# Kernel tuning notes

Hardware: AMD Instinct MI355X
Metric: run time of the kernel (lower is better)

Reference implementation:

```python
import jax, jax.numpy as jnp
import numpy as np
from jax import lax

N_CLASS, EMB, HID = 32000, 512, 1024
BATCH, SEQ = 64, 256


def _run_lstm(xs, h0, c0, Wg, Wgh, bg, Wi, Wih, bi, Wf, Wfh, bf, Wo, Woh, bo):
    # xs: [T, B, D_in]; weights stored [D_in, H] so step is x @ W (== Linear)
    def step(carry, x):
        h, c = carry
        g = jnp.tanh(x @ Wg + h @ Wgh + bg)
        i = jax.nn.sigmoid(x @ Wi + h @ Wih + bi)
        f = jax.nn.sigmoid(x @ Wf + h @ Wfh + bf)
        o = jax.nn.sigmoid(x @ Wo + h @ Woh + bo)
        c = c * f + g * i
        h = jnp.tanh(c) * o
        return (h, c), h
    (hT, cT), hs = lax.scan(step, (h0, c0), xs)
    return hs, hT


def setup_inputs() -> dict:
    key = jax.random.key(0)
    ks = jax.random.split(key, 32)
    s_e, s_h = 1.0 / np.sqrt(EMB), 1.0 / np.sqrt(HID)
    d = {}
    d["X"] = jax.random.randint(ks[0], (BATCH, SEQ), 0, N_CLASS)
    d["C"] = jax.random.normal(ks[1], (N_CLASS, EMB), jnp.float32)
    # layer 1 (input dim EMB)
    names1 = ["W1", "W_xi", "W_xf", "W_xo"]
    names1h = ["W2", "W_hi", "W_hf", "W_ho"]
    for j, n in enumerate(names1):
        d[n] = jax.random.normal(ks[2 + j], (EMB, HID), jnp.float32) * s_e
    for j, n in enumerate(names1h):
        d[n] = jax.random.normal(ks[6 + j], (HID, HID), jnp.float32) * s_h
    for n in ["b1", "b_i", "b_f", "b_o"]:
        d[n] = jnp.ones((HID,), jnp.float32)
    # layer 2 (input dim HID)
    names2 = ["W1_y", "W_xi_y", "W_xf_y", "W_xo_y", "W2_y", "W_hi_y", "W_hf_y", "W_ho_y"]
    for j, n in enumerate(names2):
        d[n] = jax.random.normal(ks[10 + j], (HID, HID), jnp.float32) * s_h
    for n in ["b1_y", "b_i_y", "b_f_y", "b_o_y"]:
        d[n] = jnp.ones((HID,), jnp.float32)
    d["W3"] = jax.random.normal(ks[20], (HID, N_CLASS), jnp.float32) * s_h
    d["b2"] = jnp.ones((N_CLASS,), jnp.float32)
    # torch code uses torch.randn initial states each call; materialize them
    d["h0"] = jax.random.normal(ks[21], (BATCH, HID), jnp.float32)
    d["c0"] = jax.random.normal(ks[22], (BATCH, HID), jnp.float32)
    d["h0_y"] = jax.random.normal(ks[23], (BATCH, HID), jnp.float32)
    d["c0_y"] = jax.random.normal(ks[24], (BATCH, HID), jnp.float32)
    return d


def reference(X, C, W1, W_xi, W_xf, W_xo, W2, W_hi, W_hf, W_ho,
              b1, b_i, b_f, b_o,
              W1_y, W_xi_y, W_xf_y, W_xo_y, W2_y, W_hi_y, W_hf_y, W_ho_y,
              b1_y, b_i_y, b_f_y, b_o_y, W3, b2, h0, c0, h0_y, c0_y):
    xs = jnp.transpose(C[X], (1, 0, 2))  # [T, B, EMB]
    hs, _ = _run_lstm(xs, h0, c0, W1, W2, b1, W_xi, W_hi, b_i,
                      W_xf, W_hf, b_f, W_xo, W_ho, b_o)
    _, hT_y = _run_lstm(hs, h0_y, c0_y, W1_y, W2_y, b1_y, W_xi_y, W_hi_y, b_i_y,
                        W_xf_y, W_hf_y, b_f_y, W_xo_y, W_ho_y, b_o_y)
    return hT_y @ W3 + b2  # [B, N_CLASS]
```

## Files before the change

kernel.cpp:

```cpp
#include <hip/hip_runtime.h>
#include <hip/hip_bf16.h>


typedef __attribute__((ext_vector_type(8))) short s16x8;
typedef __attribute__((ext_vector_type(4))) float f32x4;
typedef unsigned long long u64;

#define N_CLASS 32000
#define EMB 512
#define HID 1024
#define BATCH 64
#define SEQ 256
#define NG4 4096

#define PIN(v) asm volatile("" : "+v"(v))

static __device__ __forceinline__ short f2bf(float x) {
  __hip_bfloat16 h = __float2bfloat16(x);
  return *reinterpret_cast<short*>(&h);
}
static __device__ __forceinline__ float bf2f(short x) {
  __hip_bfloat16 h = *reinterpret_cast<__hip_bfloat16*>(&x);
  return __bfloat162float(h);
}
static __device__ __forceinline__ float fsigm(float x) {
  return __builtin_amdgcn_rcpf(1.f + __expf(-x));
}
static __device__ __forceinline__ float ftanh(float x) {
  return 2.f * __builtin_amdgcn_rcpf(1.f + __expf(-2.f * x)) - 1.f;
}

__global__ void k_conv_w4(const float* __restrict__ Wg, const float* __restrict__ Wi,
                          const float* __restrict__ Wf, const float* __restrict__ Wo,
                          short* __restrict__ sw, int K) {
  int i = blockIdx.x * 256 + threadIdx.x;
  int k8 = i >> 10, j = i & 1023;
  if (k8 >= (K >> 3)) return;
  const float* W = blockIdx.z == 0 ? Wg : blockIdx.z == 1 ? Wi : blockIdx.z == 2 ? Wf : Wo;
  s16x8 v;
#pragma unroll
  for (int e = 0; e < 8; ++e) v[e] = f2bf(W[(size_t)(k8 * 8 + e) * 1024 + j]);
  *(s16x8*)(sw + ((size_t)k8 * NG4 + blockIdx.z * 1024 + j) * 8) = v;
}

__global__ void k_bcat(const float* __restrict__ b0, const float* __restrict__ b1,
                       const float* __restrict__ b2, const float* __restrict__ b3,
                       float* __restrict__ dst) {
  int i = blockIdx.x * 256 + threadIdx.x;
  const float* s = (i >> 10) == 0 ? b0 : (i >> 10) == 1 ? b1 : (i >> 10) == 2 ? b2 : b3;
  dst[i] = s[i & 1023];
}

__global__ void k_f2bf(const float* __restrict__ src, short* __restrict__ dst, int n) {
  int i = blockIdx.x * 256 + threadIdx.x;
  if (i < n) dst[i] = f2bf(src[i]);
}

__global__ void k_embed(const int* __restrict__ X, const float* __restrict__ C,
                        short* __restrict__ xs) {
  int r = blockIdx.x;
  int t = r >> 6, b = r & 63;
  int idx = X[b * SEQ + t];
  const float* src = C + (size_t)idx * EMB;
  float2 v = *(const float2*)(src + threadIdx.x * 2);
  short* dst = xs + (size_t)r * EMB + threadIdx.x * 2;
  dst[0] = f2bf(v.x);
  dst[1] = f2bf(v.y);
}

__global__ __launch_bounds__(256) void k_gemx(const short* __restrict__ A,
                                              const short* __restrict__ Bsw,
                                              const float* __restrict__ bias,
                                              u64* __restrict__ Gsw) {
  __shared__ short lds[4096 * 8];
  int tid = threadIdx.x;
  int n0 = blockIdx.x * 64;
  for (int cid = tid; cid < 4096; cid += 256) {
    int k8 = cid >> 6, nl = cid & 63;
    *(s16x8*)(lds + (size_t)cid * 8) = *(const s16x8*)(Bsw + ((size_t)k8 * NG4 + n0 + nl) * 8);
  }
  __syncthreads();
  int lane = tid & 63, wid = tid >> 6;
  int l15 = lane & 15, l4 = lane >> 4;
  int ms = wid >> 1, ns = wid & 1;
  for (int m0 = blockIdx.y * 64; m0 < SEQ * BATCH; m0 += gridDim.y * 64) {
    f32x4 acc[2][2];
#pragma unroll
    for (int i = 0; i < 2; ++i)
#pragma unroll
      for (int j = 0; j < 2; ++j) acc[i][j] = (f32x4){0.f, 0.f, 0.f, 0.f};
    const short* a0p = A + (size_t)(m0 + ms * 32 + l15) * EMB + l4 * 8;
    const short* a1p = a0p + (size_t)16 * EMB;
#pragma unroll 4
    for (int kc = 0; kc < 16; ++kc) {
      s16x8 av0 = *(const s16x8*)(a0p + kc * 32);
      s16x8 av1 = *(const s16x8*)(a1p + kc * 32);
#pragma unroll
      for (int j = 0; j < 2; ++j) {
        s16x8 bv = *(const s16x8*)(lds + (size_t)((kc * 4 + l4) * 64 + ns * 32 + j * 16 + l15) * 8);
        acc[0][j] = __builtin_amdgcn_mfma_f32_16x16x32_bf16(av0, bv, acc[0][j], 0, 0, 0);
        acc[1][j] = __builtin_amdgcn_mfma_f32_16x16x32_bf16(av1, bv, acc[1][j], 0, 0, 0);
      }
    }
    int t = m0 >> 6;
#pragma unroll
    for (int i = 0; i < 2; ++i)
#pragma unroll
      for (int j = 0; j < 2; ++j) {
        int grp = ms * 2 + i;
        int colg = n0 + ns * 32 + j * 16 + l15;
        float bv = bias[colg];
        int q = colg >> 10, nslc = (colg >> 4) & 63;
        u64 pk = 0;
#pragma unroll
        for (int e = 0; e < 4; ++e)
          pk |= (u64)(unsigned short)f2bf(acc[i][j][e] + bv) << (16 * e);
        size_t slot = ((((size_t)t * 4 + grp) * 64 + nslc) * 4 + q) * 64 + l4 * 16 + l15;
        Gsw[slot] = pk;
      }
  }
}

__global__ __launch_bounds__(512, 2) void k_mega(
    const u64* __restrict__ G64, const short* __restrict__ Wh1sw,
    const short* __restrict__ Wx2sw, const short* __restrict__ Wh2sw,
    const float* __restrict__ bc2, u64* __restrict__ h1ex, u64* __restrict__ h2ex,
    const float* __restrict__ c0, const float* __restrict__ c0y,
    u64* __restrict__ hTy, unsigned* __restrict__ flags) {
  __shared__ short a_lds[2 * 16 * 1024];
  __shared__ f32x4 xch[8][64];
  const int tid = threadIdx.x;
  const int lane = tid & 63, W = tid >> 6;
  const int wv = W & 3, khalf = W >> 2;
  const int l15 = lane & 15, l4 = lane >> 4;
  const int xcd = (int)blockIdx.x & 7;
  const int idx = (int)blockIdx.x >> 3;
  const int group = idx & 3;
  const int nsl = ((idx >> 2) << 3) | xcd;
  const int col = (l15 >> 2) * 1024 + nsl * 16 + wv * 4 + (l15 & 3);

  s16x8 b1r[16], bxr[16], b2r[16];
#pragma unroll
  for (int j = 0; j < 16; ++j) {
    size_t o = ((size_t)((khalf * 16 + j) * 4 + l4) * NG4 + col) * 8;
    b1r[j] = *(const s16x8*)(Wh1sw + o);
    PIN(b1r[j]);
  }
#pragma unroll
  for (int j = 0; j < 16; ++j) {
    size_t o = ((size_t)((khalf * 16 + j) * 4 + l4) * NG4 + col) * 8;
    bxr[j] = *(const s16x8*)(Wx2sw + o);
    PIN(bxr[j]);
  }
#pragma unroll
  for (int j = 0; j < 16; ++j) {
    size_t o = ((size_t)((khalf * 16 + j) * 4 + l4) * NG4 + col) * 8;
    b2r[j] = *(const s16x8*)(Wh2sw + o);
    PIN(b2r[j]);
  }
  const float bias2 = bc2[col];
  float cv[4];
#pragma unroll
  for (int e = 0; e < 4; ++e) {
    int gi = (group * 16 + l4 * 4 + e) * HID + nsl * 16 + wv * 4 + (l15 & 3);
    cv[e] = (W < 4 ? c0 : c0y)[gi];
  }
  unsigned* arr = flags;
  const int srow = tid >> 5, sc5 = tid & 31;
  const int exrow = (group * 16 + srow) * 256;
  const size_t gbase =
      (((size_t)group * 64 + nsl) * 4 + (l15 >> 2)) * 64 + l4 * 16 + wv * 4 + (l15 & 3);
  u64 gcur = (W < 4) ? G64[gbase] : 0;
  u64 gnext = 0;
  const int gsrc = l4 * 16 + (l15 & 3);
  const int psrc = ((l15 >> 2) << 4) + ((l15 & 3) << 2);
  const int swzm = (l15 & 7) << 4;
  const int abase = l15 * 2048 + khalf * 1024 + l4 * 16;

  for (int r = 0; r <= 256; ++r) {
    if (W < 4 && r + 1 < 256) gnext = G64[gbase + (size_t)(r + 1) * 65536];
    if (r > 0) {
      if (tid < 64) {
        unsigned* p = arr + ((group << 6) + tid) * 32;
        while (__hip_atomic_load(p, __ATOMIC_RELAXED, __HIP_MEMORY_SCOPE_AGENT) <
               (unsigned)r)
          __builtin_amdgcn_s_sleep(1);
      }
      __syncthreads();
      asm volatile("" ::: "memory");
    }
    {
      const int slot = (r + 1) & 1;
      const u64* s1 = h1ex + slot * 16384 + exrow;
      const u64* s2 = h2ex + slot * 16384 + exrow;
#pragma unroll
      for (int i = 0; i < 8; ++i) {
        int chunk = sc5 + (i << 5);
        u64 v1 = __hip_atomic_load(s1 + chunk, __ATOMIC_RELAXED, __HIP_MEMORY_SCOPE_AGENT);
        u64 v2 = __hip_atomic_load(s2 + chunk, __ATOMIC_RELAXED, __HIP_MEMORY_SCOPE_AGENT);
        int bo = (srow * 2048 + chunk * 8) ^ ((srow & 7) << 4);
        *(u64*)((char*)a_lds + bo) = v1;
        *(u64*)((char*)a_lds + 32768 + bo) = v2;
      }
    }
    __syncthreads();

    f32x4 p1, p2a, p2b;
    if (W < 4) {
#pragma unroll
      for (int e = 0; e < 4; ++e)
        p1[e] = __uint_as_float((unsigned)((gcur >> (16 * e)) & 0xffffu) << 16);
      p2a = (f32x4){0.f, 0.f, 0.f, 0.f};
    } else {
      p1 = (f32x4){0.f, 0.f, 0.f, 0.f};
      p2a = (f32x4){bias2, bias2, bias2, bias2};
    }
    p2b = (f32x4){0.f, 0.f, 0.f, 0.f};
#pragma unroll
    for (int j = 0; j < 16; ++j) {
      int o = (abase + j * 64) ^ swzm;
      s16x8 a1 = *(const s16x8*)((const char*)a_lds + o);
      s16x8 a2 = *(const s16x8*)((const char*)a_lds + 32768 + o);
      p1 = __builtin_amdgcn_mfma_f32_16x16x32_bf16(a1, b1r[j], p1, 0, 0, 0);
      p2a = __builtin_amdgcn_mfma_f32_16x16x32_bf16(a1, bxr[j], p2a, 0, 0, 0);
      p2b = __builtin_amdgcn_mfma_f32_16x16x32_bf16(a2, b2r[j], p2b, 0, 0, 0);
    }
    f32x4 p2 = p2a + p2b;
    if (W < 4) {
      if (r >= 1) xch[W][lane] = p2;
    } else {
      if (r < 256) xch[W][lane] = p1;
    }
    __syncthreads();

    if (W < 4) {
      if (r < 256) {
        f32x4 po = xch[W + 4][lane];
        f32x4 acc = p1 + po;
        float hh0, hh1, hh2, hh3;
#pragma unroll
        for (int e = 0; e < 4; ++e) {
          float xg = __shfl(acc[e], gsrc + 0);
          float xi = __shfl(acc[e], gsrc + 4);
          float xf = __shfl(acc[e], gsrc + 8);
          float xo = __shfl(acc[e], gsrc + 12);
          float cn = cv[e] * fsigm(xf) + ftanh(xg) * fsigm(xi);
          cv[e] = cn;
          float hv = ftanh(cn) * fsigm(xo);
          if (e == 0) hh0 = hv;
          else if (e == 1) hh1 = hv;
          else if (e == 2) hh2 = hv;
          else hh3 = hv;
        }
        int rr = l15 >> 2;
        float hexp = rr == 0 ? hh0 : rr == 1 ? hh1 : rr == 2 ? hh2 : hh3;
        float p0 = __shfl(hexp, psrc + 0);
        float p1s = __shfl(hexp, psrc + 1);
        float p2s = __shfl(hexp, psrc + 2);
        float p3s = __shfl(hexp, psrc + 3);
        if (lane < 16) {
          u64 pk = (u64)(unsigned short)f2bf(p0) | ((u64)(unsigned short)f2bf(p1s) << 16) |
                   ((u64)(unsigned short)f2bf(p2s) << 32) |
                   ((u64)(unsigned short)f2bf(p3s) << 48);
          __hip_atomic_store(
              h1ex + (r & 1) * 16384 + (group * 16 + lane) * 256 + nsl * 4 + wv, pk,
              __ATOMIC_RELAXED, __HIP_MEMORY_SCOPE_AGENT);
        }
      }
    } else {
      if (r >= 1) {
        f32x4 po = xch[W - 4][lane];
        f32x4 acc = p2 + po;
        float hh0, hh1, hh2, hh3;
#pragma unroll
        for (int e = 0; e < 4; ++e) {
          float xg = __shfl(acc[e], gsrc + 0);
          float xi = __shfl(acc[e], gsrc + 4);
          float xf = __shfl(acc[e], gsrc + 8);
          float xo = __shfl(acc[e], gsrc + 12);
          float cn = cv[e] * fsigm(xf) + ftanh(xg) * fsigm(xi);
          cv[e] = cn;
          float hv = ftanh(cn) * fsigm(xo);
          if (e == 0) hh0 = hv;
          else if (e == 1) hh1 = hv;
          else if (e == 2) hh2 = hv;
          else hh3 = hv;
        }
        int rr = l15 >> 2;
        float hexp = rr == 0 ? hh0 : rr == 1 ? hh1 : rr == 2 ? hh2 : hh3;
        float p0 = __shfl(hexp, psrc + 0);
        float p1s = __shfl(hexp, psrc + 1);
        float p2s = __shfl(hexp, psrc + 2);
        float p3s = __shfl(hexp, psrc + 3);
        if (lane < 16) {
          u64 pk = (u64)(unsigned short)f2bf(p0) | ((u64)(unsigned short)f2bf(p1s) << 16) |
                   ((u64)(unsigned short)f2bf(p2s) << 32) |
                   ((u64)(unsigned short)f2bf(p3s) << 48);
          int idx2 = (group * 16 + lane) * 256 + nsl * 4 + wv;
          if (r < 256)
            __hip_atomic_store(h2ex + (r & 1) * 16384 + idx2, pk, __ATOMIC_RELAXED,
                               __HIP_MEMORY_SCOPE_AGENT);
          else
            hTy[idx2] = pk;
        }
      }
    }

    if (r < 256) {
      asm volatile("s_waitcnt vmcnt(0)" ::: "memory");
      __syncthreads();
      if (tid == 0)
        __hip_atomic_store(arr + ((group << 6) + nsl) * 32, (unsigned)(r + 1),
                           __ATOMIC_RELAXED, __HIP_MEMORY_SCOPE_AGENT);
    }
    gcur = gnext;
  }
}

__global__ __launch_bounds__(256) void k_final(const short* __restrict__ hT,
                                               const float* __restrict__ W3,
                                               float* __restrict__ partial) {
  __shared__ float hst[64][64];
  int tid = threadIdx.x;
  int n = blockIdx.x * 256 + tid;
  int kbase = blockIdx.y * 512;
  float acc[64];
#pragma unroll
  for (int i = 0; i < 64; ++i) acc[i] = 0.f;
  int bb = tid >> 2, part = tid & 3;
  for (int kc = 0; kc < 512; kc += 64) {
    __syncthreads();
    s16x8 v0 = *(const s16x8*)(hT + bb * HID + kbase + kc + part * 16);
    s16x8 v1 = *(const s16x8*)(hT + bb * HID + kbase + kc + part * 16 + 8);
#pragma unroll
    for (int e = 0; e < 8; ++e) {
      hst[part * 16 + e][bb] = bf2f(v0[e]);
      hst[part * 16 + 8 + e][bb] = bf2f(v1[e]);
    }
    __syncthreads();
    for (int k = 0; k < 64; ++k) {
      float wv = W3[(size_t)(kbase + kc + k) * N_CLASS + n];
      const float4* hp = (const float4*)&hst[k][0];
#pragma unroll
      for (int b4 = 0; b4 < 16; ++b4) {
        float4 h4 = hp[b4];
        acc[b4 * 4 + 0] += h4.x * wv;
        acc[b4 * 4 + 1] += h4.y * wv;
        acc[b4 * 4 + 2] += h4.z * wv;
        acc[b4 * 4 + 3] += h4.w * wv;
      }
    }
  }
#pragma unroll
  for (int b = 0; b < 64; ++b)
    partial[((size_t)blockIdx.y * 64 + b) * N_CLASS + n] = acc[b];
}

__global__ void k_fincomb(const float* __restrict__ partial, const float* __restrict__ b2,
                          float* __restrict__ out) {
  int n = blockIdx.x * 256 + threadIdx.x;
  int b = blockIdx.y;
  out[(size_t)b * N_CLASS + n] =
      partial[(size_t)b * N_CLASS + n] + partial[((size_t)64 + b) * N_CLASS + n] + b2[n];
}

extern "C" void kernel_launch(void* const* d_in, const int* in_sizes, int n_in, void* d_out,
                              int out_size, void* d_ws, size_t ws_size, hipStream_t stream) {
  (void)in_sizes; (void)n_in; (void)out_size; (void)ws_size;
  const int* X = (const int*)d_in[0];
  const float* C = (const float*)d_in[1];
  const float* W1 = (const float*)d_in[2];
  const float* W_xi = (const float*)d_in[3];
  const float* W_xf = (const float*)d_in[4];
  const float* W_xo = (const float*)d_in[5];
  const float* W2 = (const float*)d_in[6];
  const float* W_hi = (const float*)d_in[7];
  const float* W_hf = (const float*)d_in[8];
  const float* W_ho = (const float*)d_in[9];
  const float* b1 = (const float*)d_in[10];
  const float* b_i = (const float*)d_in[11];
  const float* b_f = (const float*)d_in[12];
  const float* b_o = (const float*)d_in[13];
  const float* W1_y = (const float*)d_in[14];
  const float* W_xi_y = (const float*)d_in[15];
  const float* W_xf_y = (const float*)d_in[16];
  const float* W_xo_y = (const float*)d_in[17];
  const float* W2_y = (const float*)d_in[18];
  const float* W_hi_y = (const float*)d_in[19];
  const float* W_hf_y = (const float*)d_in[20];
  const float* W_ho_y = (const float*)d_in[21];
  const float* b1_y = (const float*)d_in[22];
  const float* b_i_y = (const float*)d_in[23];
  const float* b_f_y = (const float*)d_in[24];
  const float* b_o_y = (const float*)d_in[25];
  const float* W3 = (const float*)d_in[26];
  const float* b2 = (const float*)d_in[27];
  const float* h0 = (const float*)d_in[28];
  const float* c0 = (const float*)d_in[29];
  const float* h0_y = (const float*)d_in[30];
  const float* c0_y = (const float*)d_in[31];

  char* w = (char*)d_ws;
  size_t off = 0;
  auto take = [&](size_t bytes) {
    char* p = w + off;
    off += (bytes + 255) & ~(size_t)255;
    return p;
  };
  short* wx1 = (short*)take(64UL * NG4 * 8 * 2);
  short* wh1 = (short*)take(128UL * NG4 * 8 * 2);
  short* wx2 = (short*)take(128UL * NG4 * 8 * 2);
  short* wh2 = (short*)take(128UL * NG4 * 8 * 2);
  short* xs = (short*)take((size_t)SEQ * BATCH * EMB * 2);
  u64* G1sw = (u64*)take((size_t)SEQ * 65536 * 8);
  float* bc1 = (float*)take(NG4 * 4);
  float* bc2 = (float*)take(NG4 * 4);
  u64* h1ex = (u64*)take(2UL * 16384 * 8);
  u64* h2ex = (u64*)take(2UL * 16384 * 8);
  u64* hTy = (u64*)take(16384UL * 8);
  unsigned* flags = (unsigned*)take(65536);

  hipMemsetAsync(flags, 0, 65536, stream);
  k_bcat<<<16, 256, 0, stream>>>(b1, b_i, b_f, b_o, bc1);
  k_bcat<<<16, 256, 0, stream>>>(b1_y, b_i_y, b_f_y, b_o_y, bc2);
  k_f2bf<<<256, 256, 0, stream>>>(h0, (short*)h1ex + 65536, BATCH * HID);
  k_f2bf<<<256, 256, 0, stream>>>(h0_y, (short*)h2ex, BATCH * HID);
  k_conv_w4<<<dim3(256, 1, 4), 256, 0, stream>>>(W1, W_xi, W_xf, W_xo, wx1, 512);
  k_conv_w4<<<dim3(512, 1, 4), 256, 0, stream>>>(W2, W_hi, W_hf, W_ho, wh1, 1024);
  k_conv_w4<<<dim3(512, 1, 4), 256, 0, stream>>>(W1_y, W_xi_y, W_xf_y, W_xo_y, wx2, 1024);
  k_conv_w4<<<dim3(512, 1, 4), 256, 0, stream>>>(W2_y, W_hi_y, W_hf_y, W_ho_y, wh2, 1024);
  k_embed<<<SEQ * BATCH, 256, 0, stream>>>(X, C, xs);
  k_gemx<<<dim3(64, 16), 256, 0, stream>>>(xs, wx1, bc1, G1sw);
  k_mega<<<256, 512, 0, stream>>>(G1sw, wh1, wx2, wh2, bc2, h1ex, h2ex, c0, c0_y, hTy,
                                  flags);
  float* partial = (float*)G1sw;
  k_final<<<dim3(125, 2), 256, 0, stream>>>((const short*)hTy, W3, partial);
  k_fincomb<<<dim3(125, 64), 256, 0, stream>>>(partial, b2, (float*)d_out);
}
```

Baseline: 2.363 ms.

## Fuse input-projection GEMM into recurrent megakernel with chunked progress flags

Folds the layer-1 input-projection GEMM (k_gemx) into the persistent LSTM kernel: 256 extra blocks compute 16-timestep chunks of the gate pre-activations and publish per-chunk progress counters. The recurrent blocks wait only on the chunk they need, so the recurrence can start before the whole projection is done and the projection overlaps the sequential steps. The grid doubles to 512 blocks with launch bounds raised to 4 blocks per CU. This relies on all blocks being co-resident to avoid deadlock and adds spin-waiting and register-pressure risk.

New measurement: 5.163 ms. 119% more time.

```diff
diff --git a/kernel.cpp b/kernel.cpp
--- a/kernel.cpp
+++ b/kernel.cpp
@@ -68,73 +68,75 @@
   dst[1] = f2bf(v.y);
 }
 
-__global__ __launch_bounds__(256) void k_gemx(const short* __restrict__ A,
-                                              const short* __restrict__ Bsw,
-                                              const float* __restrict__ bias,
-                                              u64* __restrict__ Gsw) {
-  __shared__ short lds[4096 * 8];
-  int tid = threadIdx.x;
-  int n0 = blockIdx.x * 64;
-  for (int cid = tid; cid < 4096; cid += 256) {
-    int k8 = cid >> 6, nl = cid & 63;
-    *(s16x8*)(lds + (size_t)cid * 8) = *(const s16x8*)(Bsw + ((size_t)k8 * NG4 + n0 + nl) * 8);
-  }
-  __syncthreads();
-  int lane = tid & 63, wid = tid >> 6;
-  int l15 = lane & 15, l4 = lane >> 4;
-  int ms = wid >> 1, ns = wid & 1;
-  for (int m0 = blockIdx.y * 64; m0 < SEQ * BATCH; m0 += gridDim.y * 64) {
-    f32x4 acc[2][2];
-#pragma unroll
-    for (int i = 0; i < 2; ++i)
-#pragma unroll
-      for (int j = 0; j < 2; ++j) acc[i][j] = (f32x4){0.f, 0.f, 0.f, 0.f};
-    const short* a0p = A + (size_t)(m0 + ms * 32 + l15) * EMB + l4 * 8;
-    const short* a1p = a0p + (size_t)16 * EMB;
-#pragma unroll 4
-    for (int kc = 0; kc < 16; ++kc) {
-      s16x8 av0 = *(const s16x8*)(a0p + kc * 32);
-      s16x8 av1 = *(const s16x8*)(a1p + kc * 32);
-#pragma unroll
-      for (int j = 0; j < 2; ++j) {
-        s16x8 bv = *(const s16x8*)(lds + (size_t)((kc * 4 + l4) * 64 + ns * 32 + j * 16 + l15) * 8);
-        acc[0][j] = __builtin_amdgcn_mfma_f32_16x16x32_bf16(av0, bv, acc[0][j], 0, 0, 0);
-        acc[1][j] = __builtin_amdgcn_mfma_f32_16x16x32_bf16(av1, bv, acc[1][j], 0, 0, 0);
-      }
-    }
-    int t = m0 >> 6;
-#pragma unroll
-    for (int i = 0; i < 2; ++i)
-#pragma unroll
-      for (int j = 0; j < 2; ++j) {
-        int grp = ms * 2 + i;
-        int colg = n0 + ns * 32 + j * 16 + l15;
-        float bv = bias[colg];
-        int q = colg >> 10, nslc = (colg >> 4) & 63;
-        u64 pk = 0;
-#pragma unroll
-        for (int e = 0; e < 4; ++e)
-          pk |= (u64)(unsigned short)f2bf(acc[i][j][e] + bv) << (16 * e);
-        size_t slot = ((((size_t)t * 4 + grp) * 64 + nslc) * 4 + q) * 64 + l4 * 16 + l15;
-        Gsw[slot] = pk;
-      }
-  }
-}
-
-__global__ __launch_bounds__(512, 2) void k_mega(
-    const u64* __restrict__ G64, const short* __restrict__ Wh1sw,
+__global__ __launch_bounds__(512, 4) void k_mega(
+    u64* __restrict__ G64, const short* __restrict__ Wh1sw,
     const short* __restrict__ Wx2sw, const short* __restrict__ Wh2sw,
     const float* __restrict__ bc2, u64* __restrict__ h1ex, u64* __restrict__ h2ex,
     const float* __restrict__ c0, const float* __restrict__ c0y,
-    u64* __restrict__ hTy, unsigned* __restrict__ flags) {
-  __shared__ short a_lds[2 * 16 * 1024];
-  __shared__ f32x4 xch[8][64];
+    u64* __restrict__ hTy, unsigned* __restrict__ flags,
+    const short* __restrict__ xs, const short* __restrict__ Wx1sw,
+    const float* __restrict__ bc1) {
+  __shared__ char smem[73728];
   const int tid = threadIdx.x;
   const int lane = tid & 63, W = tid >> 6;
+  const int l15 = lane & 15, l4 = lane >> 4;
+  unsigned* gprog = flags + 12288;
+
+  if ((int)blockIdx.x < 256) {
+    short* lds = (short*)smem;
+    const int n0 = ((int)blockIdx.x & 63) * 64;
+    const int mq = (int)blockIdx.x >> 6;
+    for (int cid = tid; cid < 4096; cid += 512) {
+      int k8 = cid >> 6, nl = cid & 63;
+      *(s16x8*)(lds + (size_t)cid * 8) =
+          *(const s16x8*)(Wx1sw + ((size_t)k8 * NG4 + n0 + nl) * 8);
+    }
+    __syncthreads();
+    const int ms = W >> 2, ns = W & 3;
+    const int colg = n0 + ns * 16 + l15;
+    const float bv = bc1[colg];
+    const int q = colg >> 10, nslc = (colg >> 4) & 63;
+    for (int tc = mq * 4; tc < mq * 4 + 4; ++tc) {
+      for (int mt = 0; mt < 16; ++mt) {
+        int m0 = tc * 1024 + mt * 64;
+        f32x4 acc0 = (f32x4){0.f, 0.f, 0.f, 0.f};
+        f32x4 acc1 = (f32x4){0.f, 0.f, 0.f, 0.f};
+        const short* a0p = xs + (size_t)(m0 + ms * 32 + l15) * EMB + l4 * 8;
+        const short* a1p = a0p + (size_t)16 * EMB;
+#pragma unroll 4
+        for (int kc = 0; kc < 16; ++kc) {
+          s16x8 av0 = *(const s16x8*)(a0p + kc * 32);
+          s16x8 av1 = *(const s16x8*)(a1p + kc * 32);
+          s16x8 bvv = *(const s16x8*)(lds + (size_t)((kc * 4 + l4) * 64 + ns * 16 + l15) * 8);
+          acc0 = __builtin_amdgcn_mfma_f32_16x16x32_bf16(av0, bvv, acc0, 0, 0, 0);
+          acc1 = __builtin_amdgcn_mfma_f32_16x16x32_bf16(av1, bvv, acc1, 0, 0, 0);
+        }
+        int t = m0 >> 6;
+        u64 pk0 = 0, pk1 = 0;
+#pragma unroll
+        for (int e = 0; e < 4; ++e) {
+          pk0 |= (u64)(unsigned short)f2bf(acc0[e] + bv) << (16 * e);
+          pk1 |= (u64)(unsigned short)f2bf(acc1[e] + bv) << (16 * e);
+        }
+        size_t s0 = ((((size_t)t * 4 + ms * 2) * 64 + nslc) * 4 + q) * 64 + l4 * 16 + l15;
+        G64[s0] = pk0;
+        G64[s0 + 16384] = pk1;
+      }
+      asm volatile("s_waitcnt vmcnt(0)" ::: "memory");
+      __syncthreads();
+      if (tid == 0)
+        __hip_atomic_fetch_add(gprog + tc * 32, 1u, __ATOMIC_RELEASE,
+                               __HIP_MEMORY_SCOPE_AGENT);
+    }
+    return;
+  }
+
+  const int bid2 = (int)blockIdx.x - 256;
+  short* a_lds = (short*)smem;
+  f32x4* xch = (f32x4*)(smem + 65536);
   const int wv = W & 3, khalf = W >> 2;
-  const int l15 = lane & 15, l4 = lane >> 4;
-  const int xcd = (int)blockIdx.x & 7;
-  const int idx = (int)blockIdx.x >> 3;
+  const int xcd = bid2 & 7;
+  const int idx = bid2 >> 3;
   const int group = idx & 3;
   const int nsl = ((idx >> 2) << 3) | xcd;
   const int col = (l15 >> 2) * 1024 + nsl * 16 + wv * 4 + (l15 & 3);
@@ -170,15 +172,33 @@
   const int exrow = (group * 16 + srow) * 256;
   const size_t gbase =
       (((size_t)group * 64 + nsl) * 4 + (l15 >> 2)) * 64 + l4 * 16 + wv * 4 + (l15 & 3);
-  u64 gcur = (W < 4) ? G64[gbase] : 0;
-  u64 gnext = 0;
   const int gsrc = l4 * 16 + (l15 & 3);
   const int psrc = ((l15 >> 2) << 4) + ((l15 & 3) << 2);
   const int swzm = (l15 & 7) << 4;
   const int abase = l15 * 2048 + khalf * 1024 + l4 * 16;
 
+  u64 gcur = 0, gnext = 0;
+  int readyc = -1;
+  if (W < 4) {
+    while (__hip_atomic_load(gprog, __ATOMIC_RELAXED, __HIP_MEMORY_SCOPE_AGENT) < 64u)
+      __builtin_amdgcn_s_sleep(8);
+    __builtin_amdgcn_fence(__ATOMIC_ACQUIRE, "agent");
+    readyc = 0;
+    gcur = G64[gbase];
+  }
+
   for (int r = 0; r <= 256; ++r) {
-    if (W < 4 && r + 1 < 256) gnext = G64[gbase + (size_t)(r + 1) * 65536];
+    if (W < 4 && r + 1 < 256) {
+      int nc = (r + 1) >> 4;
+      if (nc > readyc) {
+        while (__hip_atomic_load(gprog + nc * 32, __ATOMIC_RELAXED,
+                                 __HIP_MEMORY_SCOPE_AGENT) < 64u)
+          __builtin_amdgcn_s_sleep(8);
+        __builtin_amdgcn_fence(__ATOMIC_ACQUIRE, "agent");
+        readyc = nc;
+      }
+      gnext = G64[gbase + (size_t)(r + 1) * 65536];
+    }
     if (r > 0) {
       if (tid < 64) {
         unsigned* p = arr + ((group << 6) + tid) * 32;
@@ -227,15 +247,15 @@
     }
     f32x4 p2 = p2a + p2b;
     if (W < 4) {
-      if (r >= 1) xch[W][lane] = p2;
+      if (r >= 1) xch[W * 64 + lane] = p2;
     } else {
-      if (r < 256) xch[W][lane] = p1;
+      if (r < 256) xch[W * 64 + lane] = p1;
     }
     __syncthreads();
 
     if (W < 4) {
       if (r < 256) {
-        f32x4 po = xch[W + 4][lane];
+        f32x4 po = xch[(W + 4) * 64 + lane];
         f32x4 acc = p1 + po;
         float hh0, hh1, hh2, hh3;
 #pragma unroll
@@ -269,7 +289,7 @@
       }
     } else {
       if (r >= 1) {
-        f32x4 po = xch[W - 4][lane];
+        f32x4 po = xch[(W - 4) * 64 + lane];
         f32x4 acc = p2 + po;
         float hh0, hh1, hh2, hh3;
 #pragma unroll
@@ -296,12 +316,12 @@
           u64 pk = (u64)(unsigned short)f2bf(p0) | ((u64)(unsigned short)f2bf(p1s) << 16) |
                    ((u64)(unsigned short)f2bf(p2s) << 32) |
                    ((u64)(unsigned short)f2bf(p3s) << 48);
-          int idx2 = (group * 16 + lane) * 256 + nsl * 4 + wv;
+          int oidx = (group * 16 + lane) * 256 + nsl * 4 + wv;
           if (r < 256)
-            __hip_atomic_store(h2ex + (r & 1) * 16384 + idx2, pk, __ATOMIC_RELAXED,
+            __hip_atomic_store(h2ex + (r & 1) * 16384 + oidx, pk, __ATOMIC_RELAXED,
                                __HIP_MEMORY_SCOPE_AGENT);
           else
-            hTy[idx2] = pk;
+            hTy[oidx] = pk;
         }
       }
     }
@@ -430,9 +450,8 @@
   k_conv_w4<<<dim3(512, 1, 4), 256, 0, stream>>>(W1_y, W_xi_y, W_xf_y, W_xo_y, wx2, 1024);
   k_conv_w4<<<dim3(512, 1, 4), 256, 0, stream>>>(W2_y, W_hi_y, W_hf_y, W_ho_y, wh2, 1024);
   k_embed<<<SEQ * BATCH, 256, 0, stream>>>(X, C, xs);
-  k_gemx<<<dim3(64, 16), 256, 0, stream>>>(xs, wx1, bc1, G1sw);
-  k_mega<<<256, 512, 0, stream>>>(G1sw, wh1, wx2, wh2, bc2, h1ex, h2ex, c0, c0_y, hTy,
-                                  flags);
+  k_mega<<<512, 512, 0, stream>>>(G1sw, wh1, wx2, wh2, bc2, h1ex, h2ex, c0, c0_y, hTy,
+                                  flags, xs, wx1, bc1);
   float* partial = (float*)G1sw;
   k_final<<<dim3(125, 2), 256, 0, stream>>>((const short*)hTy, W3, partial);
   k_fincomb<<<dim3(125, 64), 256, 0, stream>>>(partial, b2, (float*)d_out);
```
